# Optimization experiments

Hardware: AMD Instinct MI355X
Metric: run time of the kernel (lower is better)

The kernel has to match this reference:

```python
import jax, jax.numpy as jnp
import numpy as np

EPS = 1e-9  # projective normalization epsilon
LN_EPS = 1e-5


def setup_inputs() -> dict:
    N, E, Fin, Fout = 50000, 600000, 128, 128
    key = jax.random.key(0)
    ks = jax.random.split(key, 8)
    x = jax.random.normal(ks[0], (N, Fin), jnp.float32)
    edge_index = jax.random.randint(ks[1], (2, E), 0, N, dtype=jnp.int64)
    edge_weight = jax.random.normal(ks[2], (E,), jnp.float32)
    W_self = jax.random.normal(ks[3], (Fin, Fout), jnp.float32) / np.sqrt(Fin)
    b_self = jnp.zeros((Fout,), jnp.float32)
    W_nb = jax.random.normal(ks[4], (Fin, Fout), jnp.float32) / np.sqrt(Fin)
    b_nb = jnp.zeros((Fout,), jnp.float32)
    gamma = jnp.ones((Fout,), jnp.float32)
    beta = jnp.zeros((Fout,), jnp.float32)
    return dict(x=x, edge_index=edge_index, edge_weight=edge_weight,
                W_self=W_self, b_self=b_self, W_nb=W_nb, b_nb=b_nb,
                gamma=gamma, beta=beta)


def _proj_normalize(v):
    # UHG projective_average tail: L2-normalize the weighted sum
    return v / (jnp.linalg.norm(v, axis=-1, keepdims=True) + EPS)


def reference(x, edge_index, edge_weight, W_self, b_self, W_nb, b_nb, gamma, beta):
    N = x.shape[0]
    src, tgt = edge_index[0], edge_index[1]

    # --- neighbor aggregation: per-target softmax over edge weights, then
    # weighted projective average of gathered source features (vectorized
    # replacement of the per-node python loop) ---
    seg_max = jax.ops.segment_max(edge_weight, tgt, num_segments=N)  # [N]
    ew = jnp.exp(edge_weight - seg_max[tgt])                          # [E]
    denom = jax.ops.segment_sum(ew, tgt, num_segments=N)              # [N]
    alpha = ew / denom[tgt]                                           # softmax per target
    agg = jax.ops.segment_sum(alpha[:, None] * x[src], tgt, num_segments=N)  # [N, Fin]
    agg = _proj_normalize(agg)  # isolated nodes stay exactly zero (0 / eps)

    # --- self / neighbor linear transforms ---
    self_feat = x @ W_self + b_self    # [N, Fout]
    nb_feat = agg @ W_nb + b_nb        # [N, Fout]

    # --- combine: projective average with weights [0.5, 0.5] ---
    comb = _proj_normalize(0.5 * (self_feat + nb_feat))

    # --- UHG layer norm (standard layernorm over feature dim) ---
    mu = jnp.mean(comb, axis=-1, keepdims=True)
    var = jnp.var(comb, axis=-1, keepdims=True)
    out = (comb - mu) / jnp.sqrt(var + LN_EPS) * gamma + beta
    # dropout is identity in eval mode
    return out
```

## Files before the change

kernel.cpp:

```cpp
#include <hip/hip_runtime.h>
#include <hip/hip_bf16.h>
#include <hip/hip_fp16.h>

#define EPS 1e-9f
#define LN_EPS 1e-5f

typedef __attribute__((ext_vector_type(8))) short bf16x8;
typedef __attribute__((ext_vector_type(4))) float f32x4;

__device__ __forceinline__ float lo16(unsigned p) { return __uint_as_float(p << 16); }
__device__ __forceinline__ float hi16(unsigned p) { return __uint_as_float(p & 0xffff0000u); }
__device__ __forceinline__ unsigned f2b(float f) {
    unsigned u = __float_as_uint(f);
    return (u + 0x7fffu + ((u >> 16) & 1u)) >> 16;
}
__device__ __forceinline__ int eidx(const int* ei, size_t i, int i64) {
    return i64 ? ei[2 * i] : ei[i];
}
__device__ __forceinline__ float ldw(const float* fp, const __hip_bfloat16* hp, int i, int f32) {
    return f32 ? fp[i] : __bfloat162float(hp[i]);
}

__global__ void prep(const unsigned* __restrict__ xb, const float4* __restrict__ xf4,
                     uint2* __restrict__ xcvt2, const int* __restrict__ ei,
                     const unsigned* __restrict__ Wsb, const float* __restrict__ Wsf,
                     const unsigned* __restrict__ Wnb, const float* __restrict__ Wnf,
                     unsigned* __restrict__ wt, int4* __restrict__ count4,
                     int* __restrict__ flags, int* __restrict__ ticket,
                     int n4, int zb, int N4z) {
    __shared__ int sf[2];
    if (threadIdx.x < 64) {
        int lane = threadIdx.x;
        unsigned d = xb[lane * 97];
        unsigned ex = (d >> 7) & 0xFFu;
        unsigned long long m1 = __ballot(ex >= 110u && ex <= 135u);
        int hi = ei[2 * lane + 1];
        unsigned long long m2 = __ballot(hi == 0);
        if (lane == 0) {
            sf[0] = (__popcll(m1) > 32) ? 0 : 1;
            sf[1] = (__popcll(m2) > 32) ? 1 : 0;
        }
    }
    __syncthreads();
    int f32 = sf[0];
    int b = blockIdx.x;
    if (b == 0 && threadIdx.x == 0) { flags[0] = sf[0]; flags[1] = sf[1]; }
    if (b < 64) {
        int tid = b * 256 + threadIdx.x;
        int f = tid >> 7, k2 = tid & 127;
        int k2l = k2 & 63;
        unsigned out;
        if (f32) {
            const float* W = (k2 < 64) ? Wsf : Wnf;
            float lo = W[(2 * k2l) * 128 + f], hi = W[(2 * k2l + 1) * 128 + f];
            out = f2b(lo) | (f2b(hi) << 16);
        } else {
            const unsigned* W = (k2 < 64) ? Wsb : Wnb;
            unsigned lo = W[(2 * k2l) * 64 + (f >> 1)];
            unsigned hi = W[(2 * k2l + 1) * 64 + (f >> 1)];
            unsigned a = (f & 1) ? (lo >> 16) : (lo & 0xffffu);
            unsigned b2 = (f & 1) ? (hi & 0xffff0000u) : (hi << 16);
            out = a | b2;
        }
        wt[tid] = out;
    } else if (b < 64 + zb) {
        int i = (b - 64) * 256 + threadIdx.x;
        if (i < N4z) count4[i] = make_int4(0, 0, 0, 0);
        if (b == 64 && threadIdx.x == 0) *ticket = 0;
    } else {
        if (!f32) return;
        int i = (b - 64 - zb) * 256 + threadIdx.x;
        if (i >= n4) return;
        float4 v = xf4[i];
        xcvt2[i] = make_uint2(f2b(v.x) | (f2b(v.y) << 16), f2b(v.z) | (f2b(v.w) << 16));
    }
}

__global__ void edge_count(const int* __restrict__ ei, int* __restrict__ count,
                           int* __restrict__ rank, const int* __restrict__ flags, int E) {
    int e0 = (blockIdx.x * 256 + threadIdx.x) * 4;
    if (e0 >= E) return;
    int i64 = flags[1];
    if (e0 + 4 <= E) {
        int t0, t1, t2, t3;
        if (i64 && !(E & 1)) {
            const int4* q = (const int4*)(ei + 2 * (size_t)(E + e0));
            int4 a = q[0], b = q[1];
            t0 = a.x; t1 = a.z; t2 = b.x; t3 = b.z;
        } else if (!i64 && !(E & 3)) {
            int4 a = *(const int4*)(ei + (size_t)E + e0);
            t0 = a.x; t1 = a.y; t2 = a.z; t3 = a.w;
        } else {
            t0 = eidx(ei, (size_t)E + e0 + 0, i64); t1 = eidx(ei, (size_t)E + e0 + 1, i64);
            t2 = eidx(ei, (size_t)E + e0 + 2, i64); t3 = eidx(ei, (size_t)E + e0 + 3, i64);
        }
        int r0 = atomicAdd(&count[t0], 1), r1 = atomicAdd(&count[t1], 1),
            r2 = atomicAdd(&count[t2], 1), r3 = atomicAdd(&count[t3], 1);
        *(int4*)(rank + e0) = make_int4(r0, r1, r2, r3);
    } else {
        for (int j = 0; j < 4 && e0 + j < E; ++j) {
            int t = eidx(ei, (size_t)E + e0 + j, i64);
            rank[e0 + j] = atomicAdd(&count[t], 1);
        }
    }
}

__global__ void scan_blocks(const int* __restrict__ count, int* __restrict__ offsets,
                            int* __restrict__ bsum, int* __restrict__ bpre,
                            int* __restrict__ ticket, int N, int B) {
    __shared__ int wsum[16];
    int tid = threadIdx.x, lane = tid & 63, w = tid >> 6;
    int i0 = blockIdx.x * 4096 + tid * 4;
    int4 v;
    if (i0 + 3 < N) v = *(const int4*)(count + i0);
    else {
        v.x = (i0     < N) ? count[i0]     : 0;
        v.y = (i0 + 1 < N) ? count[i0 + 1] : 0;
        v.z = (i0 + 2 < N) ? count[i0 + 2] : 0;
        v.w = (i0 + 3 < N) ? count[i0 + 3] : 0;
    }
    int s = v.x + v.y + v.z + v.w;
    int incl = s;
    #pragma unroll
    for (int off = 1; off < 64; off <<= 1) {
        int t = __shfl_up(incl, off);
        if (lane >= off) incl += t;
    }
    if (lane == 63) wsum[w] = incl;
    __syncthreads();
    int wpre = 0, tot = 0;
    #pragma unroll
    for (int j = 0; j < 16; ++j) { int sj = wsum[j]; if (j < w) wpre += sj; tot += sj; }
    int o0 = wpre + incl - s;
    int o1 = o0 + v.x, o2 = o1 + v.y, o3 = o2 + v.z;
    if (i0 + 3 < N) {
        *(int4*)(offsets + i0) = make_int4(o0, o1, o2, o3);
    } else {
        if (i0     < N) offsets[i0]     = o0;
        if (i0 + 1 < N) offsets[i0 + 1] = o1;
        if (i0 + 2 < N) offsets[i0 + 2] = o2;
    }
    if (tid == 0) {
        bsum[blockIdx.x] = tot;
        __threadfence();
        int t = atomicAdd(ticket, 1);
        if (t == B - 1) {
            int run = 0;
            for (int j = 0; j < B; ++j) {
                int vj = atomicAdd(&bsum[j], 0);
                bpre[j] = run; run += vj;
            }
            bpre[B] = run;
            offsets[N] = (N & 4095) ? (run - bpre[B - 1]) : 0;
        }
    }
}

template <int PACK>
__global__ void edge_scatter(const int* __restrict__ ei, const int* __restrict__ rank,
                             const float* __restrict__ ewf, const __hip_bfloat16* __restrict__ ewh,
                             const int* __restrict__ offsets, const int* __restrict__ bpre,
                             unsigned* __restrict__ csr4, uint2* __restrict__ csr8,
                             const int* __restrict__ flags, int E) {
    int e0 = (blockIdx.x * 256 + threadIdx.x) * 4;
    if (e0 >= E) return;
    int f32 = flags[0], i64 = flags[1];
    if (e0 + 4 <= E) {
        int4 r = *(const int4*)(rank + e0);
        int t0, t1, t2, t3, s0, s1, s2, s3;
        if (i64) {
            const int4* q = (const int4*)(ei + 2 * (size_t)e0);
            int4 a = q[0], b = q[1];
            s0 = a.x; s1 = a.z; s2 = b.x; s3 = b.z;
        } else if (!(e0 & 3)) {
            int4 a = *(const int4*)(ei + e0);
            s0 = a.x; s1 = a.y; s2 = a.z; s3 = a.w;
        } else {
            s0 = ei[e0]; s1 = ei[e0 + 1]; s2 = ei[e0 + 2]; s3 = ei[e0 + 3];
        }
        if (i64 && !(E & 1)) {
            const int4* q = (const int4*)(ei + 2 * (size_t)(E + e0));
            int4 a = q[0], b = q[1];
            t0 = a.x; t1 = a.z; t2 = b.x; t3 = b.z;
        } else if (!i64 && !(E & 3)) {
            int4 a = *(const int4*)(ei + (size_t)E + e0);
            t0 = a.x; t1 = a.y; t2 = a.z; t3 = a.w;
        } else {
            t0 = eidx(ei, (size_t)E + e0 + 0, i64); t1 = eidx(ei, (size_t)E + e0 + 1, i64);
            t2 = eidx(ei, (size_t)E + e0 + 2, i64); t3 = eidx(ei, (size_t)E + e0 + 3, i64);
        }
        float w0 = ldw(ewf, ewh, e0 + 0, f32), w1 = ldw(ewf, ewh, e0 + 1, f32),
              w2 = ldw(ewf, ewh, e0 + 2, f32), w3 = ldw(ewf, ewh, e0 + 3, f32);
        int o0 = offsets[t0] + bpre[t0 >> 12] + r.x,
            o1 = offsets[t1] + bpre[t1 >> 12] + r.y,
            o2 = offsets[t2] + bpre[t2 >> 12] + r.z,
            o3 = offsets[t3] + bpre[t3 >> 12] + r.w;
        float a0 = expf(w0), a1 = expf(w1), a2 = expf(w2), a3 = expf(w3);
        if (PACK) {
            csr4[o0] = (unsigned)s0 | ((unsigned)__half_as_ushort(__float2half(a0)) << 16);
            csr4[o1] = (unsigned)s1 | ((unsigned)__half_as_ushort(__float2half(a1)) << 16);
            csr4[o2] = (unsigned)s2 | ((unsigned)__half_as_ushort(__float2half(a2)) << 16);
            csr4[o3] = (unsigned)s3 | ((unsigned)__half_as_ushort(__float2half(a3)) << 16);
        } else {
            csr8[o0] = make_uint2((unsigned)s0, __float_as_uint(a0));
            csr8[o1] = make_uint2((unsigned)s1, __float_as_uint(a1));
            csr8[o2] = make_uint2((unsigned)s2, __float_as_uint(a2));
            csr8[o3] = make_uint2((unsigned)s3, __float_as_uint(a3));
        }
    } else {
        for (int j = 0; j < 4 && e0 + j < E; ++j) {
            int e = e0 + j;
            int t = eidx(ei, (size_t)E + e, i64);
            int s = eidx(ei, e, i64);
            float al = expf(ldw(ewf, ewh, e, f32));
            int pos = offsets[t] + bpre[t >> 12] + rank[e];
            if (PACK) csr4[pos] = (unsigned)s | ((unsigned)__half_as_ushort(__float2half(al)) << 16);
            else      csr8[pos] = make_uint2((unsigned)s, __float_as_uint(al));
        }
    }
}

template <int PACK>
__device__ __forceinline__ void dec_edge(const unsigned* __restrict__ c4,
                                         const uint2* __restrict__ c8, int j,
                                         unsigned& s, float& al) {
    if (PACK) {
        unsigned r = c4[j];
        s = r & 0xffffu;
        al = __half2float(__ushort_as_half((unsigned short)(r >> 16)));
    } else {
        uint2 e = c8[j];
        s = e.x;
        al = __uint_as_float(e.y);
    }
}

template <int PACK>
__global__ void aggregate(const unsigned* __restrict__ xb, const unsigned* __restrict__ xcvt,
                          const int* __restrict__ offsets, const int* __restrict__ bpre,
                          const unsigned* __restrict__ csr4, const uint2* __restrict__ csr8,
                          uint2* __restrict__ aggb2, const int* __restrict__ flags, int N) {
    int wid = blockIdx.x * 4 + (threadIdx.x >> 6);
    int half = (threadIdx.x >> 5) & 1;
    int node = wid * 2 + half;
    if (node >= N) return;
    int lane32 = threadIdx.x & 31;
    const uint2* xs2 = (const uint2*)(flags[0] ? xcvt : xb);
    float a0 = 0.f, a1 = 0.f, a2 = 0.f, a3 = 0.f;
    int beg = offsets[node] + bpre[node >> 12];
    int end = offsets[node + 1] + bpre[(node + 1) >> 12];
    for (int j = beg; j < end; j += 8) {
        int last = end - 1;
        int j0 = j,     i0 = (j0 < end) ? j0 : last;
        int j1 = j + 1, i1 = (j1 < end) ? j1 : last;
        int j2 = j + 2, i2 = (j2 < end) ? j2 : last;
        int j3 = j + 3, i3 = (j3 < end) ? j3 : last;
        int j4 = j + 4, i4 = (j4 < end) ? j4 : last;
        int j5 = j + 5, i5 = (j5 < end) ? j5 : last;
        int j6 = j + 6, i6 = (j6 < end) ? j6 : last;
        int j7 = j + 7, i7 = (j7 < end) ? j7 : last;
        unsigned s0, s1, s2, s3, s4, s5, s6, s7;
        float l0, l1, l2, l3, l4, l5, l6, l7;
        dec_edge<PACK>(csr4, csr8, i0, s0, l0); dec_edge<PACK>(csr4, csr8, i1, s1, l1);
        dec_edge<PACK>(csr4, csr8, i2, s2, l2); dec_edge<PACK>(csr4, csr8, i3, s3, l3);
        dec_edge<PACK>(csr4, csr8, i4, s4, l4); dec_edge<PACK>(csr4, csr8, i5, s5, l5);
        dec_edge<PACK>(csr4, csr8, i6, s6, l6); dec_edge<PACK>(csr4, csr8, i7, s7, l7);
        uint2 p0 = xs2[s0 * 32 + lane32], p1 = xs2[s1 * 32 + lane32],
              p2 = xs2[s2 * 32 + lane32], p3 = xs2[s3 * 32 + lane32],
              p4 = xs2[s4 * 32 + lane32], p5 = xs2[s5 * 32 + lane32],
              p6 = xs2[s6 * 32 + lane32], p7 = xs2[s7 * 32 + lane32];
        l1 = (j1 < end) ? l1 : 0.f; l2 = (j2 < end) ? l2 : 0.f;
        l3 = (j3 < end) ? l3 : 0.f; l4 = (j4 < end) ? l4 : 0.f;
        l5 = (j5 < end) ? l5 : 0.f; l6 = (j6 < end) ? l6 : 0.f;
        l7 = (j7 < end) ? l7 : 0.f;
        a0 += l0 * lo16(p0.x); a1 += l0 * hi16(p0.x); a2 += l0 * lo16(p0.y); a3 += l0 * hi16(p0.y);
        a0 += l1 * lo16(p1.x); a1 += l1 * hi16(p1.x); a2 += l1 * lo16(p1.y); a3 += l1 * hi16(p1.y);
        a0 += l2 * lo16(p2.x); a1 += l2 * hi16(p2.x); a2 += l2 * lo16(p2.y); a3 += l2 * hi16(p2.y);
        a0 += l3 * lo16(p3.x); a1 += l3 * hi16(p3.x); a2 += l3 * lo16(p3.y); a3 += l3 * hi16(p3.y);
        a0 += l4 * lo16(p4.x); a1 += l4 * hi16(p4.x); a2 += l4 * lo16(p4.y); a3 += l4 * hi16(p4.y);
        a0 += l5 * lo16(p5.x); a1 += l5 * hi16(p5.x); a2 += l5 * lo16(p5.y); a3 += l5 * hi16(p5.y);
        a0 += l6 * lo16(p6.x); a1 += l6 * hi16(p6.x); a2 += l6 * lo16(p6.y); a3 += l6 * hi16(p6.y);
        a0 += l7 * lo16(p7.x); a1 += l7 * hi16(p7.x); a2 += l7 * lo16(p7.y); a3 += l7 * hi16(p7.y);
    }
    float ss = a0 * a0 + a1 * a1 + a2 * a2 + a3 * a3;
    #pragma unroll
    for (int m = 16; m >= 1; m >>= 1) ss += __shfl_xor(ss, m);
    float inv = 1.f / (sqrtf(ss) + EPS);
    aggb2[node * 32 + lane32] = make_uint2(f2b(a0 * inv) | (f2b(a1 * inv) << 16),
                                           f2b(a2 * inv) | (f2b(a3 * inv) << 16));
}

__global__ __launch_bounds__(128) void fused_mfma(
    const unsigned* __restrict__ xb, const unsigned* __restrict__ xcvt,
    const unsigned* __restrict__ aggb, const uint4* __restrict__ wt4,
    const float* __restrict__ bsf, const __hip_bfloat16* __restrict__ bsh,
    const float* __restrict__ bnf, const __hip_bfloat16* __restrict__ bnh,
    const float* __restrict__ gf, const __hip_bfloat16* __restrict__ gh,
    const float* __restrict__ tf, const __hip_bfloat16* __restrict__ th,
    float* __restrict__ outf, unsigned* __restrict__ outb,
    const int* __restrict__ flags, int N)
{
    __shared__ uint4 sA[2048];
    int f32 = flags[0];
    const uint4* xs4 = (const uint4*)(f32 ? xcvt : xb);
    const uint4* ag4 = (const uint4*)aggb;
    int tid = threadIdx.x;
    int node0 = blockIdx.x * 64;

    #pragma unroll
    for (int i = 0; i < 16; ++i) {
        int ci = i * 128 + tid;
        int r = ci >> 5, c = ci & 31;
        int node = node0 + r;
        uint4 v = make_uint4(0, 0, 0, 0);
        if (node < N) v = (c < 16) ? xs4[node * 16 + c] : ag4[node * 16 + (c - 16)];
        sA[r * 32 + (c ^ (r & 15))] = v;
    }
    __syncthreads();

    int lane = tid & 63, w = tid >> 6, g = lane >> 4, c16 = lane & 15;
    int rloc0 = w * 32 + c16;
    int rloc1 = rloc0 + 16;

    f32x4 acc0[8], acc1[8];
    #pragma unroll
    for (int t = 0; t < 8; ++t) {
        acc0[t] = (f32x4){0.f, 0.f, 0.f, 0.f};
        acc1[t] = (f32x4){0.f, 0.f, 0.f, 0.f};
    }

    #pragma unroll
    for (int kk = 0; kk < 8; ++kk) {
        int cs = (kk * 4 + g) ^ c16;
        bf16x8 a0 = __builtin_bit_cast(bf16x8, sA[rloc0 * 32 + cs]);
        bf16x8 a1 = __builtin_bit_cast(bf16x8, sA[rloc1 * 32 + cs]);
        #pragma unroll
        for (int t = 0; t < 8; ++t) {
            uint4 bv = wt4[(t * 16 + c16) * 32 + kk * 4 + g];
            bf16x8 b = __builtin_bit_cast(bf16x8, bv);
            acc0[t] = __builtin_amdgcn_mfma_f32_16x16x32_bf16(a0, b, acc0[t], 0, 0, 0);
            acc1[t] = __builtin_amdgcn_mfma_f32_16x16x32_bf16(a1, b, acc1[t], 0, 0, 0);
        }
    }

    float bsum[8], gam[8], bet[8];
    #pragma unroll
    for (int t = 0; t < 8; ++t) {
        int f = t * 16 + c16;
        bsum[t] = ldw(bsf, bsh, f, f32) + ldw(bnf, bnh, f, f32);
        gam[t]  = ldw(gf, gh, f, f32);
        bet[t]  = ldw(tf, th, f, f32);
    }

    auto epilogue = [&](f32x4* acc, int rowbase) {
        #pragma unroll
        for (int reg = 0; reg < 4; ++reg) {
            int node = node0 + rowbase + g * 4 + reg;
            float cv[8], s1 = 0.f, s2 = 0.f;
            #pragma unroll
            for (int t = 0; t < 8; ++t) {
                float c_ = 0.5f * (acc[t][reg] + bsum[t]);
                cv[t] = c_; s1 += c_; s2 += c_ * c_;
            }
            #pragma unroll
            for (int m = 1; m < 16; m <<= 1) { s1 += __shfl_xor(s1, m); s2 += __shfl_xor(s2, m); }
            float inv  = 1.f / (sqrtf(s2) + EPS);
            float mean = s1 * inv * (1.f / 128.f);
            float var  = s2 * inv * inv * (1.f / 128.f) - mean * mean;
            float rstd = 1.f / sqrtf(var + LN_EPS);
            if (f32) {
                if (node < N) {
                    #pragma unroll
                    for (int t = 0; t < 8; ++t) {
                        float o = (cv[t] * inv - mean) * rstd * gam[t] + bet[t];
                        outf[(size_t)node * 128 + t * 16 + c16] = o;
                    }
                }
            } else {
                #pragma unroll
                for (int t = 0; t < 8; ++t) {
                    float o = (cv[t] * inv - mean) * rstd * gam[t] + bet[t];
                    float po = __shfl_xor(o, 1);
                    if (!(c16 & 1) && node < N)
                        outb[node * 64 + t * 8 + (c16 >> 1)] = f2b(o) | (f2b(po) << 16);
                }
            }
        }
    };
    epilogue(acc0, w * 32);
    epilogue(acc1, w * 32 + 16);
}

static inline size_t rup16(size_t x) { return (x + 15) & ~(size_t)15; }

extern "C" void kernel_launch(void* const* d_in, const int* in_sizes, int n_in,
                              void* d_out, int out_size, void* d_ws, size_t ws_size,
                              hipStream_t stream) {
    int N = in_sizes[0] / 128;
    int E = in_sizes[1] / 2;
    const int* ei = (const int*)d_in[1];

    char* p = (char*)d_ws;
    int* flags = (int*)p;              p += 16;
    int* ticket = (int*)p;             p += 16;
    int* count = (int*)p;              p += rup16((size_t)N * 4);
    int* offsets = (int*)p;            p += rup16((size_t)(N + 4) * 4);
    int* bsum = (int*)p;               p += 256;
    int* bpre = (int*)p;               p += 512;
    int* rank = (int*)p;               p += rup16((size_t)E * 4);
    unsigned* csr4 = (unsigned*)p;
    uint2* csr8 = (uint2*)p;           p += rup16((size_t)E * 8);
    unsigned* wt = (unsigned*)p;       p += 128 * 128 * 4;
    unsigned* xcvt = (unsigned*)p;     p += rup16((size_t)N * 64 * 4);
    unsigned* aggb = (unsigned*)p;

    int eb4 = (E + 1023) / 1024;
    int nb2 = (N + 7) / 8;
    int nbf = (N + 63) / 64;
    int ncv = (N * 32 + 255) / 256;
    int scanB = (N + 4095) / 4096;
    int N4z = (int)(rup16((size_t)N * 4) / 16);
    int zb = (N4z + 255) / 256;
    int pack = (N <= 65536);

    prep<<<64 + zb + ncv, 256, 0, stream>>>((const unsigned*)d_in[0], (const float4*)d_in[0],
                                            (uint2*)xcvt, ei,
                                            (const unsigned*)d_in[3], (const float*)d_in[3],
                                            (const unsigned*)d_in[5], (const float*)d_in[5],
                                            wt, (int4*)count, flags, ticket, N * 32, zb, N4z);
    edge_count<<<eb4, 256, 0, stream>>>(ei, count, rank, flags, E);
    scan_blocks<<<scanB, 1024, 0, stream>>>(count, offsets, bsum, bpre, ticket, N, scanB);
    if (pack)
        edge_scatter<1><<<eb4, 256, 0, stream>>>(ei, rank, (const float*)d_in[2],
                                                 (const __hip_bfloat16*)d_in[2],
                                                 offsets, bpre, csr4, csr8, flags, E);
    else
        edge_scatter<0><<<eb4, 256, 0, stream>>>(ei, rank, (const float*)d_in[2],
                                                 (const __hip_bfloat16*)d_in[2],
                                                 offsets, bpre, csr4, csr8, flags, E);
    if (pack)
        aggregate<1><<<nb2, 256, 0, stream>>>((const unsigned*)d_in[0], xcvt,
                                              offsets, bpre, csr4, csr8, (uint2*)aggb, flags, N);
    else
        aggregate<0><<<nb2, 256, 0, stream>>>((const unsigned*)d_in[0], xcvt,
                                              offsets, bpre, csr4, csr8, (uint2*)aggb, flags, N);
    fused_mfma<<<nbf, 128, 0, stream>>>((const unsigned*)d_in[0], xcvt, aggb, (const uint4*)wt,
                                        (const float*)d_in[4], (const __hip_bfloat16*)d_in[4],
                                        (const float*)d_in[6], (const __hip_bfloat16*)d_in[6],
                                        (const float*)d_in[7], (const __hip_bfloat16*)d_in[7],
                                        (const float*)d_in[8], (const __hip_bfloat16*)d_in[8],
                                        (float*)d_out, (unsigned*)d_out, flags, N);
}
```

Before: 195.5 us.

## Fuse edge count, scan and scatter into one cooperative kernel with grid syncs

```diff
diff --git a/kernel.cpp b/kernel.cpp
--- a/kernel.cpp
+++ b/kernel.cpp
@@ -1,6 +1,9 @@
 #include <hip/hip_runtime.h>
 #include <hip/hip_bf16.h>
 #include <hip/hip_fp16.h>
+#include <hip/hip_cooperative_groups.h>
+
+namespace cg = cooperative_groups;
 
 #define EPS 1e-9f
 #define LN_EPS 1e-5f
@@ -73,6 +76,139 @@
         if (i >= n4) return;
         float4 v = xf4[i];
         xcvt2[i] = make_uint2(f2b(v.x) | (f2b(v.y) << 16), f2b(v.z) | (f2b(v.w) << 16));
+    }
+}
+
+template <int PACK>
+__global__ __launch_bounds__(256) void edge_pipeline(
+    const int* __restrict__ ei, int* __restrict__ count, int* __restrict__ offsets,
+    int* __restrict__ bsum, int* __restrict__ bpre,
+    const float* __restrict__ ewf, const __hip_bfloat16* __restrict__ ewh,
+    unsigned* __restrict__ csr4, uint2* __restrict__ csr8,
+    const int* __restrict__ flags, int E, int N, int scanB)
+{
+    __shared__ int wsum2[4];
+    cg::grid_group grid = cg::this_grid();
+    int f32 = flags[0], i64 = flags[1];
+    int base = (blockIdx.x * 256 + threadIdx.x) * 8;
+    int t[8], s_[8], r_[8];
+    float wv[8];
+    int have = 0;
+
+    if (base < E) {
+        have = E - base; if (have > 8) have = 8;
+        if (have == 8) {
+            if (i64 && !(E & 1)) {
+                const int4* qt = (const int4*)(ei + 2 * (size_t)(E + base));
+                int4 a = qt[0], b = qt[1], c = qt[2], d = qt[3];
+                t[0]=a.x; t[1]=a.z; t[2]=b.x; t[3]=b.z; t[4]=c.x; t[5]=c.z; t[6]=d.x; t[7]=d.z;
+                const int4* qs = (const int4*)(ei + 2 * (size_t)base);
+                int4 e4 = qs[0], g4 = qs[1], h4 = qs[2], m4 = qs[3];
+                s_[0]=e4.x; s_[1]=e4.z; s_[2]=g4.x; s_[3]=g4.z; s_[4]=h4.x; s_[5]=h4.z; s_[6]=m4.x; s_[7]=m4.z;
+            } else if (!i64 && !(E & 3)) {
+                const int4* qt = (const int4*)(ei + (size_t)E + base);
+                int4 a = qt[0], b = qt[1];
+                t[0]=a.x; t[1]=a.y; t[2]=a.z; t[3]=a.w; t[4]=b.x; t[5]=b.y; t[6]=b.z; t[7]=b.w;
+                const int4* qs = (const int4*)(ei + base);
+                int4 c4 = qs[0], d4 = qs[1];
+                s_[0]=c4.x; s_[1]=c4.y; s_[2]=c4.z; s_[3]=c4.w; s_[4]=d4.x; s_[5]=d4.y; s_[6]=d4.z; s_[7]=d4.w;
+            } else {
+                #pragma unroll
+                for (int k = 0; k < 8; ++k) {
+                    t[k]  = eidx(ei, (size_t)E + base + k, i64);
+                    s_[k] = eidx(ei, (size_t)base + k, i64);
+                }
+            }
+            if (f32) {
+                const float4* qw = (const float4*)(ewf + base);
+                float4 wa = qw[0], wb = qw[1];
+                wv[0]=wa.x; wv[1]=wa.y; wv[2]=wa.z; wv[3]=wa.w;
+                wv[4]=wb.x; wv[5]=wb.y; wv[6]=wb.z; wv[7]=wb.w;
+            } else {
+                uint4 u = *(const uint4*)(ewh + base);
+                wv[0]=lo16(u.x); wv[1]=hi16(u.x); wv[2]=lo16(u.y); wv[3]=hi16(u.y);
+                wv[4]=lo16(u.z); wv[5]=hi16(u.z); wv[6]=lo16(u.w); wv[7]=hi16(u.w);
+            }
+        } else {
+            #pragma unroll
+            for (int k = 0; k < 8; ++k) if (k < have) {
+                t[k]  = eidx(ei, (size_t)E + base + k, i64);
+                s_[k] = eidx(ei, (size_t)base + k, i64);
+                wv[k] = ldw(ewf, ewh, base + k, f32);
+            }
+        }
+        #pragma unroll
+        for (int k = 0; k < 8; ++k) if (k < have) r_[k] = atomicAdd(&count[t[k]], 1);
+    }
+    __threadfence();
+    grid.sync();
+
+    if (blockIdx.x < scanB) {
+        int tid = threadIdx.x, lane = tid & 63, w = tid >> 6;
+        int i0 = blockIdx.x * 4096 + tid * 16;
+        int vv[16];
+        if (i0 + 15 < N) {
+            #pragma unroll
+            for (int q = 0; q < 4; ++q) {
+                int4 v = *(const int4*)(count + i0 + q * 4);
+                vv[q*4+0] = v.x; vv[q*4+1] = v.y; vv[q*4+2] = v.z; vv[q*4+3] = v.w;
+            }
+        } else {
+            #pragma unroll
+            for (int q = 0; q < 16; ++q) vv[q] = (i0 + q < N) ? count[i0 + q] : 0;
+        }
+        int s = 0;
+        #pragma unroll
+        for (int q = 0; q < 16; ++q) s += vv[q];
+        int incl = s;
+        #pragma unroll
+        for (int off = 1; off < 64; off <<= 1) {
+            int tt = __shfl_up(incl, off);
+            if (lane >= off) incl += tt;
+        }
+        if (lane == 63) wsum2[w] = incl;
+        __syncthreads();
+        int wpre = 0, tot = 0;
+        #pragma unroll
+        for (int j = 0; j < 4; ++j) { int sj = wsum2[j]; if (j < w) wpre += sj; tot += sj; }
+        int run = wpre + incl - s;
+        if (i0 + 15 < N) {
+            #pragma unroll
+            for (int q = 0; q < 4; ++q) {
+                int4 o;
+                o.x = run; run += vv[q*4+0];
+                o.y = run; run += vv[q*4+1];
+                o.z = run; run += vv[q*4+2];
+                o.w = run; run += vv[q*4+3];
+                *(int4*)(offsets + i0 + q * 4) = o;
+            }
+        } else {
+            #pragma unroll
+            for (int q = 0; q < 16; ++q) { if (i0 + q < N) offsets[i0 + q] = run; run += vv[q]; }
+        }
+        if (tid == 0) bsum[blockIdx.x] = tot;
+    }
+    __threadfence();
+    grid.sync();
+
+    if (blockIdx.x == 0 && threadIdx.x == 0) {
+        int run = 0;
+        for (int j = 0; j < scanB; ++j) { bpre[j] = run; run += bsum[j]; }
+        bpre[scanB] = run;
+        offsets[N] = (N & 4095) ? (run - bpre[scanB - 1]) : 0;
+    }
+    __threadfence();
+    grid.sync();
+
+    if (base < E) {
+        #pragma unroll
+        for (int k = 0; k < 8; ++k) if (k < have) {
+            int tk = t[k];
+            int pos = offsets[tk] + bpre[tk >> 12] + r_[k];
+            float al = expf(wv[k]);
+            if (PACK) csr4[pos] = (unsigned)s_[k] | ((unsigned)__half_as_ushort(__float2half(al)) << 16);
+            else      csr8[pos] = make_uint2((unsigned)s_[k], __float_as_uint(al));
+        }
     }
 }
 
@@ -428,16 +564,28 @@
                                             (const unsigned*)d_in[3], (const float*)d_in[3],
                                             (const unsigned*)d_in[5], (const float*)d_in[5],
                                             wt, (int4*)count, flags, ticket, N * 32, zb, N4z);
-    edge_count<<<eb4, 256, 0, stream>>>(ei, count, rank, flags, E);
-    scan_blocks<<<scanB, 1024, 0, stream>>>(count, offsets, bsum, bpre, ticket, N, scanB);
-    if (pack)
-        edge_scatter<1><<<eb4, 256, 0, stream>>>(ei, rank, (const float*)d_in[2],
-                                                 (const __hip_bfloat16*)d_in[2],
-                                                 offsets, bpre, csr4, csr8, flags, E);
-    else
-        edge_scatter<0><<<eb4, 256, 0, stream>>>(ei, rank, (const float*)d_in[2],
-                                                 (const __hip_bfloat16*)d_in[2],
-                                                 offsets, bpre, csr4, csr8, flags, E);
+
+    const float* ewf_ = (const float*)d_in[2];
+    const __hip_bfloat16* ewh_ = (const __hip_bfloat16*)d_in[2];
+    int ep_blocks = (E + 2047) / 2048;
+    if (ep_blocks < scanB) ep_blocks = scanB;
+    void* args[] = { (void*)&ei, (void*)&count, (void*)&offsets, (void*)&bsum, (void*)&bpre,
+                     (void*)&ewf_, (void*)&ewh_, (void*)&csr4, (void*)&csr8, (void*)&flags,
+                     (void*)&E, (void*)&N, (void*)&scanB };
+    hipError_t cerr = hipLaunchCooperativeKernel(
+        pack ? (const void*)edge_pipeline<1> : (const void*)edge_pipeline<0>,
+        dim3(ep_blocks), dim3(256), args, 0, stream);
+    if (cerr != hipSuccess) {
+        edge_count<<<eb4, 256, 0, stream>>>(ei, count, rank, flags, E);
+        scan_blocks<<<scanB, 1024, 0, stream>>>(count, offsets, bsum, bpre, ticket, N, scanB);
+        if (pack)
+            edge_scatter<1><<<eb4, 256, 0, stream>>>(ei, rank, ewf_, ewh_,
+                                                     offsets, bpre, csr4, csr8, flags, E);
+        else
+            edge_scatter<0><<<eb4, 256, 0, stream>>>(ei, rank, ewf_, ewh_,
+                                                     offsets, bpre, csr4, csr8, flags, E);
+    }
+
     if (pack)
         aggregate<1><<<nb2, 256, 0, stream>>>((const unsigned*)d_in[0], xcvt,
                                               offsets, bpre, csr4, csr8, (uint2*)aggb, flags, N);
```

Result: slower. 367.4 us (+87.9%).
